# Kernel tuning notes

Hardware: AMD Instinct MI355X
Metric: run time of the kernel (lower is better)

Reference implementation:

```python
import jax, jax.numpy as jnp
import numpy as np

B, C_IN, C_OUT, N, T = 16, 32, 64, 1024, 24
IN_DIM, S_DIM, D_DIM, K, KT = 1, 16, 16, 3, 3


def conv1x1(x, W, b):
    # x: [B,Ci,N,T], W: [Co,Ci], b: [Co] -> [B,Co,N,T]
    return jnp.einsum('oi,bint->bont', W, x) + b[None, :, None, None]


def conv_t(x, W, b):
    # temporal conv, kernel (1,KT), padding (0,1) -> length preserved
    out = jax.lax.conv_general_dilated(
        x, W, window_strides=(1, 1), padding=((0, 0), (1, 1)),
        dimension_numbers=('NCHW', 'OIHW', 'NCHW'))
    return out + b[None, :, None, None]


def coss_attn(Dv, y, Wq, bq, Wk, bk, Wv, bv):
    # cross-attention per node over the temporal axis: Q from y, K/V from Dv
    Q = conv1x1(y, Wq, bq)
    Kx = conv1x1(Dv, Wk, bk)
    V = conv1x1(Dv, Wv, bv)
    scale = 1.0 / jnp.sqrt(jnp.asarray(Q.shape[1], Q.dtype))
    A = jax.nn.softmax(jnp.einsum('bcnt,bcns->bnts', Q, Kx) * scale, axis=-1)
    return jnp.einsum('bnts,bcns->bcnt', A, V)


def cheby(x, supports, Wg, bg, k):
    # Chebyshev polynomial graph conv: T0=I, T1=L, T2=2L T1 - T0
    n = supports.shape[0]
    L0 = jnp.eye(n, dtype=x.dtype)
    L1 = supports
    Ls = [L0, L1]
    for _ in range(2, k):
        L2 = 2.0 * supports @ L1 - L0
        L0, L1 = L1, L2
        Ls.append(L2)
    Lap = jnp.stack(Ls, 0)  # [K,N,N]
    xk = jnp.einsum('kqn,bcnt->bckqt', Lap, x)  # aggregate neighbours
    bsz, c, kk, nn, tt = xk.shape
    xk = xk.reshape(bsz, c * kk, nn, tt)
    return conv1x1(xk, Wg, bg)


def setup_inputs() -> dict:
    key = jax.random.key(0)
    ks = jax.random.split(key, 32)
    s = 0.05
    inp = {
        'x': jax.random.normal(ks[0], (B, C_IN, N, T), jnp.float32),
        'supports': jax.random.normal(ks[1], (N, N), jnp.float32) / np.sqrt(N).astype(np.float32),
        'CD': jax.random.normal(ks[2], (N, D_DIM), jnp.float32),
        'CS': jax.random.normal(ks[3], (N, S_DIM), jnp.float32),
        'adj': jax.random.normal(ks[4], (N, N), jnp.float32) / np.sqrt(N).astype(np.float32),
        # DelayEstimators params
        'W_de': jax.random.normal(ks[5], (C_OUT, C_IN), jnp.float32) * s,
        'b_de': jnp.zeros((C_OUT,), jnp.float32),
        'Wd': jax.random.normal(ks[6], (D_DIM, T), jnp.float32) * s,
        # conv_pro
        'W_pro': jax.random.normal(ks[7], (IN_DIM, C_IN), jnp.float32) * s,
        'b_pro': jnp.zeros((IN_DIM,), jnp.float32),
        # MultiScaleGCN
        'W_mii': jax.random.normal(ks[8], (C_OUT, S_DIM), jnp.float32) * s,
        'b_mii': jnp.zeros((C_OUT,), jnp.float32),
        # conv_1 residual
        'W_1': jax.random.normal(ks[9], (C_OUT, C_IN), jnp.float32) * s,
        'b_1': jnp.zeros((C_OUT,), jnp.float32),
        # TSFN cross-attention (query from x with c_in channels)
        'Wq_t': jax.random.normal(ks[10], (C_OUT, C_IN), jnp.float32) * s,
        'bq_t': jnp.zeros((C_OUT,), jnp.float32),
        'Wk_t': jax.random.normal(ks[11], (C_OUT, C_OUT), jnp.float32) * s,
        'bk_t': jnp.zeros((C_OUT,), jnp.float32),
        'Wv_t': jax.random.normal(ks[12], (C_OUT, C_OUT), jnp.float32) * s,
        'bv_t': jnp.zeros((C_OUT,), jnp.float32),
        # conv1 temporal (1,Kt)
        'W_c1': jax.random.normal(ks[13], (C_OUT, C_OUT, 1, KT), jnp.float32) * s,
        'b_c1': jnp.zeros((C_OUT,), jnp.float32),
        # SSFN cross-attention
        'Wq_s': jax.random.normal(ks[14], (C_OUT, C_OUT), jnp.float32) * s,
        'bq_s': jnp.zeros((C_OUT,), jnp.float32),
        'Wk_s': jax.random.normal(ks[15], (C_OUT, C_OUT), jnp.float32) * s,
        'bk_s': jnp.zeros((C_OUT,), jnp.float32),
        'Wv_s': jax.random.normal(ks[16], (C_OUT, C_OUT), jnp.float32) * s,
        'bv_s': jnp.zeros((C_OUT,), jnp.float32),
        # cheby conv output projection (K*c_out -> 2*c_out)
        'W_g': jax.random.normal(ks[17], (2 * C_OUT, K * C_OUT), jnp.float32) * s,
        'b_g': jnp.zeros((2 * C_OUT,), jnp.float32),
    }
    return inp


def reference(x, supports, CD, CS, adj, W_de, b_de, Wd, W_pro, b_pro,
              W_mii, b_mii, W_1, b_1, Wq_t, bq_t, Wk_t, bk_t, Wv_t, bv_t,
              W_c1, b_c1, Wq_s, bq_s, Wk_s, bk_s, Wv_s, bv_s, W_g, b_g):
    # DelayEstimators: projected trend modulated by node-wise learned delay gate
    delay = jax.nn.sigmoid(jnp.tanh(CD @ Wd))            # [N,T]
    D = conv1x1(x, W_de, b_de) * delay[None, None, :, :]  # [B,c_out,N,T]
    # conv_pro + broadcast of spatial context CS
    u = conv1x1(x, W_pro, b_pro)[:, 0]                    # [B,N,T] (in_dim==1)
    CSb = jnp.einsum('bnt,ne->bent', u, CS)               # [B,S_dim,N,T]
    # MultiScaleGCN: 1x1 projection + adjacency aggregation (identity + adj)
    h = conv1x1(CSb, W_mii, b_mii)
    S = h + jnp.einsum('nm,bcmt->bcnt', adj, h)           # [B,c_out,N,T]
    x_input1 = conv1x1(x, W_1, b_1)
    XD = coss_attn(D, x, Wq_t, bq_t, Wk_t, bk_t, Wv_t, bv_t) + x_input1
    x1 = conv_t(XD, W_c1, b_c1)
    XS = coss_attn(S, x1, Wq_s, bq_s, Wk_s, bk_s, Wv_s, bv_s)
    x2 = cheby(XS, supports, W_g, b_g, K)                 # [B,2*c_out,N,T]
    filt, gate = x2[:, :C_OUT], x2[:, C_OUT:]
    return (filt + x_input1) * jax.nn.sigmoid(gate)
```

## Files before the change

### kernel.cpp

```cpp
#include <hip/hip_runtime.h>
#include <cstdint>
#include <cstddef>

#define B_    16
#define CIN_  32
#define COUT_ 64
#define N_    1024
#define T_    24
#define SD_   16
#define DD_   16

#define NT_      (N_*T_)
#define BNT_     (B_*N_*T_)
#define UE_COLS  (B_*T_*SD_)
#define XS_COLS  (B_*COUT_*T_)
#define HALF_COLS (XS_COLS/2)

typedef unsigned short ushort_t;
using bf16x8 = __attribute__((ext_vector_type(8))) short;
using f32x4  = __attribute__((ext_vector_type(4))) float;

#define OFF_DELAY 0ul
#define OFF_M     98304ul
#define OFF_R     360448ul
#define OFF_U     364544ul
#define OFF_W1T   1953792ul
#define OFF_WGBF  2048000ul
#define OFF_WGT   2097152ul
#define OFF_SBF   2195456ul
#define OFF_ADJBF 4292608ul
#define OFF_STBF  6389760ul
#define OFF_L2BF  8486912ul
#define OFF_X1    10584064ul
#define OFF_X2    23166976ul
#define OFF_XS    48332800ul
#define OFF_Y1H   98664448ul
#define OFF_Y2H   123830272ul
#define OFF_WBF   148996096ul

#define WB_DE   0
#define WB_QT   2048
#define WB_1    4096
#define WB_MIIA 6144
#define WB_KT   8192
#define WB_VT   12288
#define WB_QS   16384
#define WB_KS   20480
#define WB_VS   24576
#define WB_C1A  28672
#define WB_TOTAL 40960

__device__ __forceinline__ float bfb2f(ushort_t h) {
  union { unsigned u; float f; } v; v.u = ((unsigned)h) << 16; return v.f;
}
__device__ __forceinline__ ushort_t f2bfb(float f) {
  union { float f; unsigned u; } v; v.f = f;
  unsigned u = v.u;
  return (ushort_t)((u + 0x7fffu + ((u >> 16) & 1u)) >> 16);
}
__device__ __forceinline__ float sigm_(float z) { return 1.f / (1.f + expf(-z)); }

__device__ __forceinline__ void gl_lds16(const ushort_t* g, ushort_t* l) {
  __builtin_amdgcn_global_load_lds(
      (const __attribute__((address_space(1))) unsigned int*)g,
      (__attribute__((address_space(3))) unsigned int*)l, 16, 0, 0);
}

__device__ __forceinline__ void st4bf(ushort_t* p, float v0, float v1, float v2, float v3) {
  uint2 w;
  w.x = (unsigned)f2bfb(v0) | ((unsigned)f2bfb(v1) << 16);
  w.y = (unsigned)f2bfb(v2) | ((unsigned)f2bfb(v3) << 16);
  *(uint2*)p = w;
}

__global__ __launch_bounds__(256) void k_prep(
    const float* __restrict__ supports, const float* __restrict__ adj,
    const float* __restrict__ W_de, const float* __restrict__ Wq_t,
    const float* __restrict__ W_1, const float* __restrict__ W_mii,
    const float* __restrict__ Wk_t, const float* __restrict__ Wv_t,
    const float* __restrict__ Wq_s, const float* __restrict__ Wk_s,
    const float* __restrict__ Wv_s, const float* __restrict__ W_c1,
    const float* __restrict__ W_g,
    ushort_t* __restrict__ Sbf, ushort_t* __restrict__ adjbf,
    ushort_t* __restrict__ STbf,
    float* __restrict__ W1T, ushort_t* __restrict__ WGBF,
    ushort_t* __restrict__ WBF)
{
  int idx = blockIdx.x * 256 + threadIdx.x;
  if (idx < N_*N_) {
    Sbf[idx]   = f2bfb(supports[idx]);
    adjbf[idx] = f2bfb(adj[idx]);
    int n = idx >> 10, k = idx & 1023;
    STbf[idx]  = f2bfb(supports[k*N_ + n]);
  }
  int j = idx - N_*N_;
  if (j < 0) return;
  if (j < 2048) { int k = j>>6, c = j&63; W1T[j] = W_1[c*32 + k]; return; }
  j -= 2048;
  if (j < 24576) { WGBF[j] = f2bfb(W_g[j]); return; }
  j -= 24576;
  if (j < 2048) { WBF[WB_DE + j] = f2bfb(W_de[j]); return; }
  j -= 2048;
  if (j < 2048) { WBF[WB_QT + j] = f2bfb(Wq_t[j]); return; }
  j -= 2048;
  if (j < 2048) { WBF[WB_1 + j] = f2bfb(W_1[j]); return; }
  j -= 2048;
  if (j < 2048) { int c = j>>5, k = j&31;
                  WBF[WB_MIIA + j] = (k < 16) ? f2bfb(W_mii[c*16 + k]) : (ushort_t)0; return; }
  j -= 2048;
  if (j < 4096) { WBF[WB_KT + j] = f2bfb(Wk_t[j]); return; }
  j -= 4096;
  if (j < 4096) { WBF[WB_VT + j] = f2bfb(Wv_t[j]); return; }
  j -= 4096;
  if (j < 4096) { WBF[WB_QS + j] = f2bfb(Wq_s[j]); return; }
  j -= 4096;
  if (j < 4096) { WBF[WB_KS + j] = f2bfb(Wk_s[j]); return; }
  j -= 4096;
  if (j < 4096) { WBF[WB_VS + j] = f2bfb(Wv_s[j]); return; }
  j -= 4096;
  if (j < 12288) { int d = j >> 12, r = j & 4095, c = r >> 6, jj = r & 63;
                   WBF[WB_C1A + j] = f2bfb(W_c1[(c*64 + jj)*3 + d]); return; }
}
#define PREP_TOTAL (N_*N_ + 2048 + 24576 + WB_TOTAL)

__global__ __launch_bounds__(256) void k_pre(
    const float* __restrict__ CD, const float* __restrict__ Wd,
    const float* __restrict__ CS, const float* __restrict__ W_mii,
    const float* __restrict__ adj,
    float* __restrict__ delay, float* __restrict__ Mbuf, float* __restrict__ Rbuf)
{
  int idx = blockIdx.x * 256 + threadIdx.x;
  if (idx < NT_) {
    int n = idx / T_, t = idx % T_;
    float z = 0.f;
    #pragma unroll
    for (int d = 0; d < DD_; ++d) z += CD[n*DD_ + d] * Wd[d*T_ + t];
    delay[idx] = sigm_(tanhf(z));
  }
  int i2 = idx - NT_;
  if (i2 >= 0 && i2 < N_*COUT_) {
    int n = i2 / COUT_, c = i2 % COUT_;
    float z = 0.f;
    #pragma unroll
    for (int e = 0; e < SD_; ++e) z += CS[n*SD_ + e] * W_mii[c*SD_ + e];
    Mbuf[i2] = z;
  }
  int i3 = idx - NT_ - N_*COUT_;
  if (i3 >= 0 && i3 < N_) {
    const float* row = adj + (size_t)i3 * N_;
    float s = 0.f;
    for (int m = 0; m < N_; ++m) s += row[m];
    Rbuf[i3] = s;
  }
}

__global__ __launch_bounds__(256) void k_u(
    const float* __restrict__ x, const float* __restrict__ W_pro,
    const float* __restrict__ b_pro, const float* __restrict__ CS,
    float* __restrict__ u, ushort_t* __restrict__ Ue)
{
  int idx = blockIdx.x * 256 + threadIdx.x;
  if (idx >= BNT_) return;
  int t = idx % T_;
  int n = (idx / T_) % N_;
  int b = idx / (T_ * N_);
  const float* xp = x + ((size_t)b * CIN_ * N_ + n) * T_ + t;
  float z = b_pro[0];
  #pragma unroll
  for (int i = 0; i < CIN_; ++i) z += W_pro[i] * xp[(size_t)i * NT_];
  u[idx] = z;
  ushort_t* up = Ue + (size_t)n * UE_COLS + (b * T_ + t) * SD_;
  #pragma unroll
  for (int e = 0; e < SD_; ++e) up[e] = f2bfb(z * CS[n*SD_ + e]);
}

__global__ __launch_bounds__(256) void k_tr(
    const ushort_t* __restrict__ src, ushort_t* __restrict__ dst,
    int R, int sstride)
{
  __shared__ ushort_t tb[32][33];
  const int tid = threadIdx.x;
  const int tx = tid & 31, ty = tid >> 5;
  const int c0 = blockIdx.x * 32, r0 = blockIdx.y * 32;
  #pragma unroll
  for (int p = 0; p < 4; ++p) {
    int r = r0 + ty + p*8;
    tb[ty + p*8][tx] = src[(size_t)r * sstride + c0 + tx];
  }
  __syncthreads();
  #pragma unroll
  for (int p = 0; p < 4; ++p) {
    int c = c0 + ty + p*8;
    dst[(size_t)c * R + r0 + tx] = tb[tx][ty + p*8];
  }
}

template<int MODE>
__global__ __launch_bounds__(256) void k_mmx(
    const ushort_t* __restrict__ Abf, const ushort_t* __restrict__ BT,
    ushort_t* __restrict__ Cc, int ncols)
{
  __shared__ ushort_t As[128*64];
  __shared__ ushort_t Bs[128*64];
  const int tid  = threadIdx.x;
  const int wave = tid >> 6, lane = tid & 63;
  const int row0 = blockIdx.y * 128;
  const int col0 = blockIdx.x * 128;
  const int wm = (wave >> 1) * 64, wn = (wave & 1) * 64;
  const int l15 = lane & 15, quad = lane >> 4, l7 = lane & 7;

  f32x4 acc[4][4];
  #pragma unroll
  for (int i = 0; i < 4; ++i)
    #pragma unroll
    for (int j = 0; j < 4; ++j) acc[i][j] = (f32x4){0.f,0.f,0.f,0.f};

  for (int kb = 0; kb < 1024; kb += 64) {
    #pragma unroll
    for (int p = 0; p < 4; ++p) {
      int chunk = p*256 + tid;
      int r = chunk >> 3, pc = chunk & 7;
      int kc = pc ^ (r & 7);
      gl_lds16(Abf + (size_t)(row0 + r)*1024 + (kb + kc*8), &As[chunk*8]);
    }
    #pragma unroll
    for (int p = 0; p < 4; ++p) {
      int chunk = p*256 + tid;
      int r = chunk >> 3, pc = chunk & 7;
      int kc = pc ^ (r & 7);
      gl_lds16(BT + (size_t)(col0 + r)*1024 + (kb + kc*8), &Bs[chunk*8]);
    }
    __syncthreads();
    #pragma unroll
    for (int kh = 0; kh < 2; ++kh) {
      const int kcb = kh * 4;
      bf16x8 af[4], bfr[4];
      #pragma unroll
      for (int mi = 0; mi < 4; ++mi)
        af[mi] = *(const bf16x8*)&As[(wm + mi*16 + l15)*64 + (((kcb + quad) ^ l7) << 3)];
      #pragma unroll
      for (int ni = 0; ni < 4; ++ni)
        bfr[ni] = *(const bf16x8*)&Bs[(wn + ni*16 + l15)*64 + (((kcb + quad) ^ l7) << 3)];
      #pragma unroll
      for (int mi = 0; mi < 4; ++mi)
        #pragma unroll
        for (int ni = 0; ni < 4; ++ni)
          acc[mi][ni] = __builtin_amdgcn_mfma_f32_16x16x32_bf16(
              af[mi], bfr[ni], acc[mi][ni], 0, 0, 0);
    }
    __syncthreads();
  }

  #pragma unroll
  for (int mi = 0; mi < 4; ++mi) {
    int grow_b = row0 + wm + mi*16 + quad*4;
    #pragma unroll
    for (int ni = 0; ni < 4; ++ni) {
      int gcol = col0 + wn + ni*16 + l15;
      #pragma unroll
      for (int j = 0; j < 4; ++j) {
        float v = acc[mi][ni][j];
        int grow = grow_b + j;
        if (MODE == 2) v = 2.f*v - ((grow == gcol) ? 1.f : 0.f);
        Cc[(size_t)grow * ncols + gcol] = f2bfb(v);
      }
    }
  }
}

#define SW 72
__global__ __launch_bounds__(256) void k_attn_mfma(
    const float* __restrict__ x,
    const float* __restrict__ delay, const float* __restrict__ Mbuf,
    const float* __restrict__ Rbuf, const float* __restrict__ u,
    const ushort_t* __restrict__ P,
    const ushort_t* __restrict__ WBF,
    const float* __restrict__ b_de, const float* __restrict__ bq_t,
    const float* __restrict__ b_1,  const float* __restrict__ b_mii,
    const float* __restrict__ bk_t, const float* __restrict__ bv_t,
    const float* __restrict__ bq_s, const float* __restrict__ bk_s,
    const float* __restrict__ bv_s, const float* __restrict__ b_c1,
    ushort_t* __restrict__ XS)
{
  const int n = blockIdx.x, b = blockIdx.y;
  const int tid = threadIdx.x, wave = tid >> 6, lane = tid & 63;
  const int l15 = lane & 15, quad = lane >> 4;

  __shared__ __align__(16) char smem[31520];
  ushort_t* bufQ = (ushort_t*)(smem + 0);
  ushort_t* XDg  = (ushort_t*)(smem + 0);
  ushort_t* Bc   = (ushort_t*)(smem + 4896);
  ushort_t* bufK = (ushort_t*)(smem + 4896);
  ushort_t* scb  = (ushort_t*)(smem + 4896);
  ushort_t* Pts  = (ushort_t*)(smem + 9504);
  float*    scf  = (float*)(smem + 9504);
  ushort_t* bufD = (ushort_t*)(smem + 12064);
  ushort_t* x1s  = (ushort_t*)(smem + 16672);
  ushort_t* Sts  = (ushort_t*)(smem + 21280);
  ushort_t* V2   = (ushort_t*)(smem + 25888);
  float* delay_s = (float*)(smem + 31008);
  float* urow    = (float*)(smem + 31136);
  float* Mrow    = (float*)(smem + 31264);

  for (int i = tid; i < 768; i += 256) {
    int ci = i / 24, t = i - ci*24;
    Bc[t*SW + ci] = f2bfb(x[(((size_t)b*CIN_ + ci)*N_ + n)*T_ + t]);
  }
  for (int i = tid; i < 768; i += 256) {
    int t = i >> 5, e = i & 31;
    Pts[t*40 + e] = (e < 16) ? P[(size_t)n*UE_COLS + (b*T_ + t)*SD_ + e] : (ushort_t)0;
  }
  if (tid < 32)       urow[tid] = (tid < 24) ? u[((size_t)b*N_ + n)*T_ + tid] : 0.f;
  else if (tid < 64)  { int t = tid - 32; delay_s[t] = (t < 24) ? delay[n*T_ + t] : 0.f; }
  else if (tid < 128) Mrow[tid - 64] = Mbuf[n*COUT_ + (tid - 64)];
  for (int i = tid; i < 64*40; i += 256) V2[i] = 0;
  __syncthreads();

  const int c0 = wave * 16;
  const float Rn = Rbuf[n];

  {
    bf16x8 aD = *(const bf16x8*)(WBF + WB_DE   + (c0+l15)*32 + quad*8);
    bf16x8 aQ = *(const bf16x8*)(WBF + WB_QT   + (c0+l15)*32 + quad*8);
    bf16x8 a1 = *(const bf16x8*)(WBF + WB_1    + (c0+l15)*32 + quad*8);
    bf16x8 aS = *(const bf16x8*)(WBF + WB_MIIA + (c0+l15)*32 + quad*8);
    float4 bD4 = *(const float4*)&b_de [c0 + quad*4];
    float4 bQ4 = *(const float4*)&bq_t [c0 + quad*4];
    float4 b14 = *(const float4*)&b_1  [c0 + quad*4];
    float4 bS4 = *(const float4*)&b_mii[c0 + quad*4];
    float4 Mv4 = *(const float4*)&Mrow [c0 + quad*4];
    float bD[4] = {bD4.x,bD4.y,bD4.z,bD4.w};
    float bQ[4] = {bQ4.x,bQ4.y,bQ4.z,bQ4.w};
    float b1a[4] = {b14.x,b14.y,b14.z,b14.w};
    float bS[4] = {bS4.x,bS4.y,bS4.z,bS4.w};
    float Mv[4] = {Mv4.x,Mv4.y,Mv4.z,Mv4.w};
    #pragma unroll
    for (int nt = 0; nt < 2; ++nt) {
      int bt = nt*16 + l15;
      bf16x8 bx = *(const bf16x8*)&Bc[bt*SW + quad*8];
      bf16x8 bp = *(const bf16x8*)&Pts[bt*40 + quad*8];
      f32x4 z = {0.f,0.f,0.f,0.f};
      f32x4 accD = __builtin_amdgcn_mfma_f32_16x16x32_bf16(aD, bx, z, 0,0,0);
      f32x4 accQ = __builtin_amdgcn_mfma_f32_16x16x32_bf16(aQ, bx, z, 0,0,0);
      f32x4 acc1 = __builtin_amdgcn_mfma_f32_16x16x32_bf16(a1, bx, z, 0,0,0);
      f32x4 accS = __builtin_amdgcn_mfma_f32_16x16x32_bf16(aS, bp, z, 0,0,0);
      float dl = delay_s[bt], ut = urow[bt];
      st4bf(&bufD[bt*SW + c0 + quad*4],
            (accD[0]+bD[0])*dl, (accD[1]+bD[1])*dl, (accD[2]+bD[2])*dl, (accD[3]+bD[3])*dl);
      st4bf(&bufQ[bt*SW + c0 + quad*4],
            accQ[0]+bQ[0], accQ[1]+bQ[1], accQ[2]+bQ[2], accQ[3]+bQ[3]);
      st4bf(&x1s[bt*SW + c0 + quad*4],
            acc1[0]+b1a[0], acc1[1]+b1a[1], acc1[2]+b1a[2], acc1[3]+b1a[3]);
      st4bf(&Sts[bt*SW + c0 + quad*4],
            accS[0] + ut*Mv[0] + bS[0]*(1.f+Rn), accS[1] + ut*Mv[1] + bS[1]*(1.f+Rn),
            accS[2] + ut*Mv[2] + bS[2]*(1.f+Rn), accS[3] + ut*Mv[3] + bS[3]*(1.f+Rn));
    }
  }
  __syncthreads();

  {
    bf16x8 aK0 = *(const bf16x8*)(WBF + WB_KT + (c0+l15)*64 + quad*8);
    bf16x8 aK1 = *(const bf16x8*)(WBF + WB_KT + (c0+l15)*64 + 32 + quad*8);
    bf16x8 aV0 = *(const bf16x8*)(WBF + WB_VT + (c0+l15)*64 + quad*8);
    bf16x8 aV1 = *(const bf16x8*)(WBF + WB_VT + (c0+l15)*64 + 32 + quad*8);
    float4 bK4 = *(const float4*)&bk_t[c0 + quad*4];
    float4 bV4 = *(const float4*)&bv_t[c0 + quad*4];
    float bK[4] = {bK4.x,bK4.y,bK4.z,bK4.w};
    float bV[4] = {bV4.x,bV4.y,bV4.z,bV4.w};
    #pragma unroll
    for (int nt = 0; nt < 2; ++nt) {
      int bt = nt*16 + l15;
      bf16x8 b0 = *(const bf16x8*)&bufD[bt*SW + quad*8];
      bf16x8 b1v = *(const bf16x8*)&bufD[bt*SW + 32 + quad*8];
      f32x4 accK = {0.f,0.f,0.f,0.f}, accV = {0.f,0.f,0.f,0.f};
      accK = __builtin_amdgcn_mfma_f32_16x16x32_bf16(aK0, b0,  accK, 0,0,0);
      accK = __builtin_amdgcn_mfma_f32_16x16x32_bf16(aK1, b1v, accK, 0,0,0);
      accV = __builtin_amdgcn_mfma_f32_16x16x32_bf16(aV0, b0,  accV, 0,0,0);
      accV = __builtin_amdgcn_mfma_f32_16x16x32_bf16(aV1, b1v, accV, 0,0,0);
      st4bf(&bufK[bt*SW + c0 + quad*4],
            accK[0]+bK[0], accK[1]+bK[1], accK[2]+bK[2], accK[3]+bK[3]);
      if (bt < 24) {
        #pragma unroll
        for (int r = 0; r < 4; ++r)
          V2[(c0 + quad*4 + r)*40 + bt] = f2bfb(accV[r] + bV[r]);
      }
    }
  }
  __syncthreads();

  {
    int mt = (wave >> 1) * 16, ns = (wave & 1) * 16;
    bf16x8 a0 = *(const bf16x8*)&bufQ[(mt+l15)*SW + quad*8];
    bf16x8 a1f = *(const bf16x8*)&bufQ[(mt+l15)*SW + 32 + quad*8];
    bf16x8 b0 = *(const bf16x8*)&bufK[(ns+l15)*SW + quad*8];
    bf16x8 b1f = *(const bf16x8*)&bufK[(ns+l15)*SW + 32 + quad*8];
    f32x4 acc = {0.f,0.f,0.f,0.f};
    acc = __builtin_amdgcn_mfma_f32_16x16x32_bf16(a0, b0, acc, 0,0,0);
    acc = __builtin_amdgcn_mfma_f32_16x16x32_bf16(a1f, b1f, acc, 0,0,0);
    int s = ns + l15;
    if (s < 24) {
      #pragma unroll
      for (int r = 0; r < 4; ++r) {
        int t = mt + quad*4 + r;
        if (t < 24) scf[t*25 + s] = 0.125f * acc[r];
      }
    }
  }
  __syncthreads();

  {
    int t = tid >> 3, j = tid & 7;
    if (t < 24) {
      float v0 = scf[t*25 + j], v1 = scf[t*25 + j + 8], v2 = scf[t*25 + j + 16];
      float mx = fmaxf(fmaxf(v0, v1), v2);
      mx = fmaxf(mx, __shfl_xor(mx, 1));
      mx = fmaxf(mx, __shfl_xor(mx, 2));
      mx = fmaxf(mx, __shfl_xor(mx, 4));
      float e0 = expf(v0 - mx), e1 = expf(v1 - mx), e2 = expf(v2 - mx);
      float sm = e0 + e1 + e2;
      sm += __shfl_xor(sm, 1);
      sm += __shfl_xor(sm, 2);
      sm += __shfl_xor(sm, 4);
      float inv = 1.f / sm;
      scb[t*40 + j]      = f2bfb(e0 * inv);
      scb[t*40 + j + 8]  = f2bfb(e1 * inv);
      scb[t*40 + j + 16] = f2bfb(e2 * inv);
      scb[t*40 + 24 + j] = 0;
    }
  }
  __syncthreads();

  {
    for (int i = tid; i < 640; i += 256) {
      int r = i >> 6, cg = i & 63;
      int row = (r == 0) ? 0 : (24 + r);
      XDg[row*SW + cg] = 0;
    }
    int nc = wave * 16;
    bf16x8 bv0 = *(const bf16x8*)&V2[(nc + l15)*40 + quad*8];
    #pragma unroll
    for (int mt = 0; mt < 2; ++mt) {
      bf16x8 af = *(const bf16x8*)&scb[(mt*16 + l15)*40 + quad*8];
      f32x4 acc = {0.f,0.f,0.f,0.f};
      acc = __builtin_amdgcn_mfma_f32_16x16x32_bf16(af, bv0, acc, 0,0,0);
      int ccol = nc + l15;
      #pragma unroll
      for (int r = 0; r < 4; ++r) {
        int t = mt*16 + quad*4 + r;
        if (t < 24)
          XDg[(1 + t)*SW + ccol] = f2bfb(acc[r] + bfb2f(x1s[t*SW + ccol]));
      }
    }
  }
  __syncthreads();

  {
    float4 bc4 = *(const float4*)&b_c1[c0 + quad*4];
    float bc[4] = {bc4.x,bc4.y,bc4.z,bc4.w};
    f32x4 acc0 = {0.f,0.f,0.f,0.f}, acc1v = {0.f,0.f,0.f,0.f};
    #pragma unroll
    for (int d = 0; d < 3; ++d) {
      const ushort_t* Ad = WBF + WB_C1A + d*4096;
      bf16x8 a0 = *(const bf16x8*)(Ad + (c0+l15)*64 + quad*8);
      bf16x8 a1f = *(const bf16x8*)(Ad + (c0+l15)*64 + 32 + quad*8);
      {
        int rr = 0*16 + l15 + d;
        bf16x8 b0 = *(const bf16x8*)&XDg[rr*SW + quad*8];
        bf16x8 b1f = *(const bf16x8*)&XDg[rr*SW + 32 + quad*8];
        acc0 = __builtin_amdgcn_mfma_f32_16x16x32_bf16(a0, b0, acc0, 0,0,0);
        acc0 = __builtin_amdgcn_mfma_f32_16x16x32_bf16(a1f, b1f, acc0, 0,0,0);
      }
      {
        int rr = 1*16 + l15 + d;
        bf16x8 b0 = *(const bf16x8*)&XDg[rr*SW + quad*8];
        bf16x8 b1f = *(const bf16x8*)&XDg[rr*SW + 32 + quad*8];
        acc1v = __builtin_amdgcn_mfma_f32_16x16x32_bf16(a0, b0, acc1v, 0,0,0);
        acc1v = __builtin_amdgcn_mfma_f32_16x16x32_bf16(a1f, b1f, acc1v, 0,0,0);
      }
    }
    st4bf(&bufD[(0*16 + l15)*SW + c0 + quad*4],
          acc0[0]+bc[0], acc0[1]+bc[1], acc0[2]+bc[2], acc0[3]+bc[3]);
    st4bf(&bufD[(1*16 + l15)*SW + c0 + quad*4],
          acc1v[0]+bc[0], acc1v[1]+bc[1], acc1v[2]+bc[2], acc1v[3]+bc[3]);
  }
  __syncthreads();

  {
    bf16x8 aq0 = *(const bf16x8*)(WBF + WB_QS + (c0+l15)*64 + quad*8);
    bf16x8 aq1 = *(const bf16x8*)(WBF + WB_QS + (c0+l15)*64 + 32 + quad*8);
    bf16x8 ak0 = *(const bf16x8*)(WBF + WB_KS + (c0+l15)*64 + quad*8);
    bf16x8 ak1 = *(const bf16x8*)(WBF + WB_KS + (c0+l15)*64 + 32 + quad*8);
    bf16x8 av0 = *(const bf16x8*)(WBF + WB_VS + (c0+l15)*64 + quad*8);
    bf16x8 av1 = *(const bf16x8*)(WBF + WB_VS + (c0+l15)*64 + 32 + quad*8);
    float4 bq4 = *(const float4*)&bq_s[c0 + quad*4];
    float4 bk4 = *(const float4*)&bk_s[c0 + quad*4];
    float4 bv4 = *(const float4*)&bv_s[c0 + quad*4];
    float bq[4] = {bq4.x,bq4.y,bq4.z,bq4.w};
    float bk[4] = {bk4.x,bk4.y,bk4.z,bk4.w};
    float bv[4] = {bv4.x,bv4.y,bv4.z,bv4.w};
    #pragma unroll
    for (int nt = 0; nt < 2; ++nt) {
      int bt = nt*16 + l15;
      bf16x8 bx0 = *(const bf16x8*)&bufD[bt*SW + quad*8];
      bf16x8 bx1 = *(const bf16x8*)&bufD[bt*SW + 32 + quad*8];
      bf16x8 bs0 = *(const bf16x8*)&Sts[bt*SW + quad*8];
      bf16x8 bs1 = *(const bf16x8*)&Sts[bt*SW + 32 + quad*8];
      f32x4 accQ = {0.f,0.f,0.f,0.f}, accK = {0.f,0.f,0.f,0.f}, accV = {0.f,0.f,0.f,0.f};
      accQ = __builtin_amdgcn_mfma_f32_16x16x32_bf16(aq0, bx0, accQ, 0,0,0);
      accQ = __builtin_amdgcn_mfma_f32_16x16x32_bf16(aq1, bx1, accQ, 0,0,0);
      accK = __builtin_amdgcn_mfma_f32_16x16x32_bf16(ak0, bs0, accK, 0,0,0);
      accK = __builtin_amdgcn_mfma_f32_16x16x32_bf16(ak1, bs1, accK, 0,0,0);
      accV = __builtin_amdgcn_mfma_f32_16x16x32_bf16(av0, bs0, accV, 0,0,0);
      accV = __builtin_amdgcn_mfma_f32_16x16x32_bf16(av1, bs1, accV, 0,0,0);
      st4bf(&bufQ[bt*SW + c0 + quad*4],
            accQ[0]+bq[0], accQ[1]+bq[1], accQ[2]+bq[2], accQ[3]+bq[3]);
      st4bf(&bufK[bt*SW + c0 + quad*4],
            accK[0]+bk[0], accK[1]+bk[1], accK[2]+bk[2], accK[3]+bk[3]);
      if (bt < 24) {
        #pragma unroll
        for (int r = 0; r < 4; ++r)
          V2[(c0 + quad*4 + r)*40 + bt] = f2bfb(accV[r] + bv[r]);
      }
    }
  }
  __syncthreads();

  {
    int mt = (wave >> 1) * 16, ns = (wave & 1) * 16;
    bf16x8 a0 = *(const bf16x8*)&bufQ[(mt+l15)*SW + quad*8];
    bf16x8 a1f = *(const bf16x8*)&bufQ[(mt+l15)*SW + 32 + quad*8];
    bf16x8 b0 = *(const bf16x8*)&bufK[(ns+l15)*SW + quad*8];
    bf16x8 b1f = *(const bf16x8*)&bufK[(ns+l15)*SW + 32 + quad*8];
    f32x4 acc = {0.f,0.f,0.f,0.f};
    acc = __builtin_amdgcn_mfma_f32_16x16x32_bf16(a0, b0, acc, 0,0,0);
    acc = __builtin_amdgcn_mfma_f32_16x16x32_bf16(a1f, b1f, acc, 0,0,0);
    int s = ns + l15;
    if (s < 24) {
      #pragma unroll
      for (int r = 0; r < 4; ++r) {
        int t = mt + quad*4 + r;
        if (t < 24) scf[t*25 + s] = 0.125f * acc[r];
      }
    }
  }
  __syncthreads();

  {
    int t = tid >> 3, j = tid & 7;
    if (t < 24) {
      float v0 = scf[t*25 + j], v1 = scf[t*25 + j + 8], v2 = scf[t*25 + j + 16];
      float mx = fmaxf(fmaxf(v0, v1), v2);
      mx = fmaxf(mx, __shfl_xor(mx, 1));
      mx = fmaxf(mx, __shfl_xor(mx, 2));
      mx = fmaxf(mx, __shfl_xor(mx, 4));
      float e0 = expf(v0 - mx), e1 = expf(v1 - mx), e2 = expf(v2 - mx);
      float sm = e0 + e1 + e2;
      sm += __shfl_xor(sm, 1);
      sm += __shfl_xor(sm, 2);
      sm += __shfl_xor(sm, 4);
      float inv = 1.f / sm;
      scb[t*40 + j]      = f2bfb(e0 * inv);
      scb[t*40 + j + 8]  = f2bfb(e1 * inv);
      scb[t*40 + j + 16] = f2bfb(e2 * inv);
      scb[t*40 + 24 + j] = 0;
    }
  }
  __syncthreads();

  {
    int nc = wave * 16;
    bf16x8 bv0 = *(const bf16x8*)&V2[(nc + l15)*40 + quad*8];
    #pragma unroll
    for (int mt = 0; mt < 2; ++mt) {
      bf16x8 af = *(const bf16x8*)&scb[(mt*16 + l15)*40 + quad*8];
      f32x4 acc = {0.f,0.f,0.f,0.f};
      acc = __builtin_amdgcn_mfma_f32_16x16x32_bf16(af, bv0, acc, 0,0,0);
      int ccol = nc + l15;
      int t0 = mt*16 + quad*4;
      if (t0 < 24) {
        uint2 w;
        w.x = (unsigned)f2bfb(acc[0]) | ((unsigned)f2bfb(acc[1]) << 16);
        w.y = (unsigned)f2bfb(acc[2]) | ((unsigned)f2bfb(acc[3]) << 16);
        *(uint2*)(XS + (size_t)n*XS_COLS + (size_t)b*COUT_*T_ + ccol*T_ + t0) = w;
      }
    }
  }
}

#define ZW 200
__global__ __launch_bounds__(256) void k_final(
    const float* __restrict__ x,
    const ushort_t* __restrict__ XS, const ushort_t* __restrict__ Y1h,
    const ushort_t* __restrict__ Y2h,
    const ushort_t* __restrict__ WGBF,
    const float* __restrict__ W1T, const float* __restrict__ b_1,
    const float* __restrict__ b_g,
    int h, float* __restrict__ out)
{
  const int n = blockIdx.x, bb = blockIdx.y, tid = threadIdx.x;
  const int b = h * 8 + bb;
  const int wave = tid >> 6, lane = tid & 63;
  const int l15 = lane & 15, quad = lane >> 4;

  __shared__ __align__(16) ushort_t Zt[32*ZW];
  __shared__ float x1sh[COUT_*T_];
  __shared__ float xts[CIN_*T_];

  size_t baseg = (size_t)n * XS_COLS + (size_t)b * COUT_ * T_;
  size_t baseh = (size_t)n * HALF_COLS + (size_t)bb * COUT_ * T_;

  for (int i = tid; i < 8*ZW; i += 256) Zt[24*ZW + i] = 0;
  for (int i = tid; i < COUT_*T_; i += 256) {
    int c = i / T_, t = i - c*T_;
    ushort_t* zr = &Zt[t*ZW + 3*c];
    zr[0] = XS [baseg + i];
    zr[1] = Y1h[baseh + i];
    zr[2] = Y2h[baseh + i];
  }
  for (int i = tid; i < CIN_*T_; i += 256) {
    int ci = i / T_, t = i - ci*T_;
    xts[i] = x[(((size_t)b * CIN_ + ci) * N_ + n) * T_ + t];
  }
  __syncthreads();

  {
    const int c = tid >> 2, tq = tid & 3;
    float a[6];
    #pragma unroll
    for (int m = 0; m < 6; ++m) a[m] = b_1[c];
    for (int i = 0; i < CIN_; ++i) {
      float w = W1T[i*64 + c];
      #pragma unroll
      for (int m = 0; m < 6; ++m) a[m] += w * xts[i*T_ + tq + 4*m];
    }
    #pragma unroll
    for (int m = 0; m < 6; ++m) x1sh[c*T_ + tq + 4*m] = a[m];
  }

  f32x4 accF[2] = {{0.f,0.f,0.f,0.f},{0.f,0.f,0.f,0.f}};
  f32x4 accG[2] = {{0.f,0.f,0.f,0.f},{0.f,0.f,0.f,0.f}};
  const ushort_t* WF = WGBF + (size_t)(wave*16 + l15)*192 + quad*8;
  const ushort_t* WG = WF + 64*192;
  #pragma unroll
  for (int ks = 0; ks < 6; ++ks) {
    bf16x8 wf = *(const bf16x8*)(WF + ks*32);
    bf16x8 wg = *(const bf16x8*)(WG + ks*32);
    #pragma unroll
    for (int nt = 0; nt < 2; ++nt) {
      bf16x8 bz = *(const bf16x8*)&Zt[(nt*16 + l15)*ZW + ks*32 + quad*8];
      accF[nt] = __builtin_amdgcn_mfma_f32_16x16x32_bf16(wf, bz, accF[nt], 0,0,0);
      accG[nt] = __builtin_amdgcn_mfma_f32_16x16x32_bf16(wg, bz, accG[nt], 0,0,0);
    }
  }
  __syncthreads();

  {
    float4 bgF4 = *(const float4*)&b_g[wave*16 + quad*4];
    float4 bgG4 = *(const float4*)&b_g[64 + wave*16 + quad*4];
    float bgF[4] = {bgF4.x, bgF4.y, bgF4.z, bgF4.w};
    float bgG[4] = {bgG4.x, bgG4.y, bgG4.z, bgG4.w};
    #pragma unroll
    for (int nt = 0; nt < 2; ++nt) {
      int t = nt*16 + l15;
      if (t < 24) {
        #pragma unroll
        for (int r = 0; r < 4; ++r) {
          int c = wave*16 + quad*4 + r;
          float fv = accF[nt][r] + bgF[r] + x1sh[c*T_ + t];
          float gv = accG[nt][r] + bgG[r];
          out[(((size_t)b * COUT_ + c) * N_ + n) * T_ + t] = fv * sigm_(gv);
        }
      }
    }
  }
}

extern "C" void kernel_launch(void* const* d_in, const int* in_sizes, int n_in,
                              void* d_out, int out_size, void* d_ws, size_t ws_size,
                              hipStream_t stream) {
  const float* x        = (const float*)d_in[0];
  const float* supports = (const float*)d_in[1];
  const float* CD       = (const float*)d_in[2];
  const float* CS       = (const float*)d_in[3];
  const float* adj      = (const float*)d_in[4];
  const float* W_de  = (const float*)d_in[5];  const float* b_de  = (const float*)d_in[6];
  const float* Wd    = (const float*)d_in[7];
  const float* W_pro = (const float*)d_in[8];  const float* b_pro = (const float*)d_in[9];
  const float* W_mii = (const float*)d_in[10]; const float* b_mii = (const float*)d_in[11];
  const float* W_1   = (const float*)d_in[12]; const float* b_1   = (const float*)d_in[13];
  const float* Wq_t  = (const float*)d_in[14]; const float* bq_t  = (const float*)d_in[15];
  const float* Wk_t  = (const float*)d_in[16]; const float* bk_t  = (const float*)d_in[17];
  const float* Wv_t  = (const float*)d_in[18]; const float* bv_t  = (const float*)d_in[19];
  const float* W_c1  = (const float*)d_in[20]; const float* b_c1  = (const float*)d_in[21];
  const float* Wq_s  = (const float*)d_in[22]; const float* bq_s  = (const float*)d_in[23];
  const float* Wk_s  = (const float*)d_in[24]; const float* bk_s  = (const float*)d_in[25];
  const float* Wv_s  = (const float*)d_in[26]; const float* bv_s  = (const float*)d_in[27];
  const float* W_g   = (const float*)d_in[28]; const float* b_g   = (const float*)d_in[29];
  float* out = (float*)d_out;

  char* ws = (char*)d_ws;
  float*    delay = (float*)(ws + OFF_DELAY);
  float*    Mbuf  = (float*)(ws + OFF_M);
  float*    Rbuf  = (float*)(ws + OFF_R);
  float*    u     = (float*)(ws + OFF_U);
  float*    W1T   = (float*)(ws + OFF_W1T);
  ushort_t* WGBF  = (ushort_t*)(ws + OFF_WGBF);
  ushort_t* Sbf   = (ushort_t*)(ws + OFF_SBF);
  ushort_t* adjbf = (ushort_t*)(ws + OFF_ADJBF);
  ushort_t* STbf  = (ushort_t*)(ws + OFF_STBF);
  ushort_t* L2bf  = (ushort_t*)(ws + OFF_L2BF);
  ushort_t* Ue    = (ushort_t*)(ws + OFF_X1);
  ushort_t* P     = (ushort_t*)(ws + OFF_X1);
  ushort_t* UeT   = (ushort_t*)(ws + OFF_X2);
  ushort_t* XST   = (ushort_t*)(ws + OFF_X2);
  ushort_t* XS    = (ushort_t*)(ws + OFF_XS);
  ushort_t* Y1h   = (ushort_t*)(ws + OFF_Y1H);
  ushort_t* Y2h   = (ushort_t*)(ws + OFF_Y2H);
  ushort_t* WBF   = (ushort_t*)(ws + OFF_WBF);

  (void)in_sizes; (void)n_in; (void)out_size; (void)ws_size;

  k_prep<<<dim3((PREP_TOTAL + 255)/256), 256, 0, stream>>>(
      supports, adj, W_de, Wq_t, W_1, W_mii, Wk_t, Wv_t, Wq_s, Wk_s, Wv_s,
      W_c1, W_g, Sbf, adjbf, STbf, W1T, WGBF, WBF);
  k_pre<<<dim3((NT_ + N_*COUT_ + N_ + 255)/256), 256, 0, stream>>>(
      CD, Wd, CS, W_mii, adj, delay, Mbuf, Rbuf);
  k_mmx<2><<<dim3(8, 8), 256, 0, stream>>>(Sbf, STbf, L2bf, 1024);
  k_u<<<dim3((BNT_ + 255)/256), 256, 0, stream>>>(x, W_pro, b_pro, CS, u, Ue);
  k_tr<<<dim3(UE_COLS/32, N_/32), 256, 0, stream>>>(Ue, UeT, N_, UE_COLS);
  k_mmx<0><<<dim3(UE_COLS/128, N_/128), 256, 0, stream>>>(adjbf, UeT, P, UE_COLS);
  k_attn_mfma<<<dim3(N_, B_), 256, 0, stream>>>(
      x, delay, Mbuf, Rbuf, u, P, WBF,
      b_de, bq_t, b_1, b_mii, bk_t, bv_t, bq_s, bk_s, bv_s, b_c1, XS);
  for (int h = 0; h < 2; ++h) {
    k_tr<<<dim3(HALF_COLS/32, N_/32), 256, 0, stream>>>(
        XS + (size_t)h * HALF_COLS, XST, N_, XS_COLS);
    k_mmx<0><<<dim3(HALF_COLS/128, N_/128), 256, 0, stream>>>(Sbf, XST, Y1h, HALF_COLS);
    k_mmx<0><<<dim3(HALF_COLS/128, N_/128), 256, 0, stream>>>(L2bf, XST, Y2h, HALF_COLS);
    k_final<<<dim3(N_, 8), 256, 0, stream>>>(
        x, XS, Y1h, Y2h, WGBF, W1T, b_1, b_g, h, out);
  }
}
```

Measured before the change: 799.9 us.

## Merge Chebyshev GEMMs, restructure attention softmax in registers, shrink LDS footprint

The two per-half Chebyshev GEMMs (S and L2 against XST) are merged into one launch, with grid.y choosing the A matrix, which cuts launches and improves tail fill. Both attention stages now compute the 24x24 scores in two waves with the softmax done in registers via shuffles, removing an fp32 score buffer in shared memory and one barrier. The x_input1 term is held in registers instead of LDS, and the shared buffers are re-aliased so each block uses less LDS, with launch bounds raised to allow more resident blocks. The supports transpose moves from a strided gather in prep to the existing tiled transpose kernel, and the adj row sums are split across 8 lanes. Risks are more register pressure and two idle waves during the score step.

```diff
diff --git a/kernel.cpp b/kernel.cpp
--- a/kernel.cpp
+++ b/kernel.cpp
@@ -26,7 +26,6 @@
 #define OFF_U     364544ul
 #define OFF_W1T   1953792ul
 #define OFF_WGBF  2048000ul
-#define OFF_WGT   2097152ul
 #define OFF_SBF   2195456ul
 #define OFF_ADJBF 4292608ul
 #define OFF_STBF  6389760ul
@@ -82,7 +81,6 @@
     const float* __restrict__ Wv_s, const float* __restrict__ W_c1,
     const float* __restrict__ W_g,
     ushort_t* __restrict__ Sbf, ushort_t* __restrict__ adjbf,
-    ushort_t* __restrict__ STbf,
     float* __restrict__ W1T, ushort_t* __restrict__ WGBF,
     ushort_t* __restrict__ WBF)
 {
@@ -90,8 +88,6 @@
   if (idx < N_*N_) {
     Sbf[idx]   = f2bfb(supports[idx]);
     adjbf[idx] = f2bfb(adj[idx]);
-    int n = idx >> 10, k = idx & 1023;
-    STbf[idx]  = f2bfb(supports[k*N_ + n]);
   }
   int j = idx - N_*N_;
   if (j < 0) return;
@@ -146,11 +142,15 @@
     Mbuf[i2] = z;
   }
   int i3 = idx - NT_ - N_*COUT_;
-  if (i3 >= 0 && i3 < N_) {
-    const float* row = adj + (size_t)i3 * N_;
+  if (i3 >= 0 && i3 < 8*N_) {
+    int n = i3 >> 3, jl = i3 & 7;
+    const float* row = adj + (size_t)n * N_;
     float s = 0.f;
-    for (int m = 0; m < N_; ++m) s += row[m];
-    Rbuf[i3] = s;
+    for (int m = jl; m < N_; m += 8) s += row[m];
+    s += __shfl_xor(s, 1);
+    s += __shfl_xor(s, 2);
+    s += __shfl_xor(s, 4);
+    if (jl == 0) Rbuf[n] = s;
   }
 }
 
@@ -268,8 +268,80 @@
   }
 }
 
+__global__ __launch_bounds__(256) void k_mmy(
+    const ushort_t* __restrict__ Sbf, const ushort_t* __restrict__ L2bf,
+    const ushort_t* __restrict__ BT,
+    ushort_t* __restrict__ Y1, ushort_t* __restrict__ Y2, int ncols)
+{
+  __shared__ ushort_t As[128*64];
+  __shared__ ushort_t Bs[128*64];
+  const int tid  = threadIdx.x;
+  const int wave = tid >> 6, lane = tid & 63;
+  const bool isY2 = blockIdx.y >= 8;
+  const ushort_t* Abf = isY2 ? L2bf : Sbf;
+  ushort_t* Cc = isY2 ? Y2 : Y1;
+  const int row0 = (blockIdx.y & 7) * 128;
+  const int col0 = blockIdx.x * 128;
+  const int wm = (wave >> 1) * 64, wn = (wave & 1) * 64;
+  const int l15 = lane & 15, quad = lane >> 4, l7 = lane & 7;
+
+  f32x4 acc[4][4];
+  #pragma unroll
+  for (int i = 0; i < 4; ++i)
+    #pragma unroll
+    for (int j = 0; j < 4; ++j) acc[i][j] = (f32x4){0.f,0.f,0.f,0.f};
+
+  for (int kb = 0; kb < 1024; kb += 64) {
+    #pragma unroll
+    for (int p = 0; p < 4; ++p) {
+      int chunk = p*256 + tid;
+      int r = chunk >> 3, pc = chunk & 7;
+      int kc = pc ^ (r & 7);
+      gl_lds16(Abf + (size_t)(row0 + r)*1024 + (kb + kc*8), &As[chunk*8]);
+    }
+    #pragma unroll
+    for (int p = 0; p < 4; ++p) {
+      int chunk = p*256 + tid;
+      int r = chunk >> 3, pc = chunk & 7;
+      int kc = pc ^ (r & 7);
+      gl_lds16(BT + (size_t)(col0 + r)*1024 + (kb + kc*8), &Bs[chunk*8]);
+    }
+    __syncthreads();
+    #pragma unroll
+    for (int kh = 0; kh < 2; ++kh) {
+      const int kcb = kh * 4;
+      bf16x8 af[4], bfr[4];
+      #pragma unroll
+      for (int mi = 0; mi < 4; ++mi)
+        af[mi] = *(const bf16x8*)&As[(wm + mi*16 + l15)*64 + (((kcb + quad) ^ l7) << 3)];
+      #pragma unroll
+      for (int ni = 0; ni < 4; ++ni)
+        bfr[ni] = *(const bf16x8*)&Bs[(wn + ni*16 + l15)*64 + (((kcb + quad) ^ l7) << 3)];
+      #pragma unroll
+      for (int mi = 0; mi < 4; ++mi)
+        #pragma unroll
+        for (int ni = 0; ni < 4; ++ni)
+          acc[mi][ni] = __builtin_amdgcn_mfma_f32_16x16x32_bf16(
+              af[mi], bfr[ni], acc[mi][ni], 0, 0, 0);
+    }
+    __syncthreads();
+  }
+
+  #pragma unroll
+  for (int mi = 0; mi < 4; ++mi) {
+    int grow_b = row0 + wm + mi*16 + quad*4;
+    #pragma unroll
+    for (int ni = 0; ni < 4; ++ni) {
+      int gcol = col0 + wn + ni*16 + l15;
+      #pragma unroll
+      for (int j = 0; j < 4; ++j)
+        Cc[(size_t)(grow_b + j) * ncols + gcol] = f2bfb(acc[mi][ni][j]);
+    }
+  }
+}
+
 #define SW 72
-__global__ __launch_bounds__(256) void k_attn_mfma(
+__global__ __launch_bounds__(256, 6) void k_attn_mfma(
     const float* __restrict__ x,
     const float* __restrict__ delay, const float* __restrict__ Mbuf,
     const float* __restrict__ Rbuf, const float* __restrict__ u,
@@ -286,21 +358,19 @@
   const int tid = threadIdx.x, wave = tid >> 6, lane = tid & 63;
   const int l15 = lane & 15, quad = lane >> 4;
 
-  __shared__ __align__(16) char smem[31520];
+  __shared__ __align__(16) char smem[24352];
   ushort_t* bufQ = (ushort_t*)(smem + 0);
   ushort_t* XDg  = (ushort_t*)(smem + 0);
   ushort_t* Bc   = (ushort_t*)(smem + 4896);
   ushort_t* bufK = (ushort_t*)(smem + 4896);
-  ushort_t* scb  = (ushort_t*)(smem + 4896);
-  ushort_t* Pts  = (ushort_t*)(smem + 9504);
-  float*    scf  = (float*)(smem + 9504);
-  ushort_t* bufD = (ushort_t*)(smem + 12064);
-  ushort_t* x1s  = (ushort_t*)(smem + 16672);
-  ushort_t* Sts  = (ushort_t*)(smem + 21280);
-  ushort_t* V2   = (ushort_t*)(smem + 25888);
-  float* delay_s = (float*)(smem + 31008);
-  float* urow    = (float*)(smem + 31136);
-  float* Mrow    = (float*)(smem + 31264);
+  ushort_t* bufD = (ushort_t*)(smem + 9504);
+  ushort_t* scb  = (ushort_t*)(smem + 9504);
+  ushort_t* Sts  = (ushort_t*)(smem + 14112);
+  ushort_t* V2   = (ushort_t*)(smem + 18720);
+  ushort_t* Pts  = (ushort_t*)(smem + 18720);
+  float* delay_s = (float*)(smem + 23840);
+  float* urow    = (float*)(smem + 23968);
+  float* Mrow    = (float*)(smem + 24096);
 
   for (int i = tid; i < 768; i += 256) {
     int ci = i / 24, t = i - ci*24;
@@ -313,16 +383,16 @@
   if (tid < 32)       urow[tid] = (tid < 24) ? u[((size_t)b*N_ + n)*T_ + tid] : 0.f;
   else if (tid < 64)  { int t = tid - 32; delay_s[t] = (t < 24) ? delay[n*T_ + t] : 0.f; }
   else if (tid < 128) Mrow[tid - 64] = Mbuf[n*COUT_ + (tid - 64)];
-  for (int i = tid; i < 64*40; i += 256) V2[i] = 0;
   __syncthreads();
 
   const int c0 = wave * 16;
   const float Rn = Rbuf[n];
+  float x1r[2][4];
 
   {
     bf16x8 aD = *(const bf16x8*)(WBF + WB_DE   + (c0+l15)*32 + quad*8);
     bf16x8 aQ = *(const bf16x8*)(WBF + WB_QT   + (c0+l15)*32 + quad*8);
-    bf16x8 a1 = *(const bf16x8*)(WBF + WB_1    + (c0+l15)*32 + quad*8);
+    bf16x8 a1w = *(const bf16x8*)(WBF + WB_1   + (c0+l15)*32 + quad*8);
     bf16x8 aS = *(const bf16x8*)(WBF + WB_MIIA + (c0+l15)*32 + quad*8);
     float4 bD4 = *(const float4*)&b_de [c0 + quad*4];
     float4 bQ4 = *(const float4*)&bq_t [c0 + quad*4];
@@ -342,15 +412,15 @@
       f32x4 z = {0.f,0.f,0.f,0.f};
       f32x4 accD = __builtin_amdgcn_mfma_f32_16x16x32_bf16(aD, bx, z, 0,0,0);
       f32x4 accQ = __builtin_amdgcn_mfma_f32_16x16x32_bf16(aQ, bx, z, 0,0,0);
-      f32x4 acc1 = __builtin_amdgcn_mfma_f32_16x16x32_bf16(a1, bx, z, 0,0,0);
+      f32x4 acc1 = __builtin_amdgcn_mfma_f32_16x16x32_bf16(a1w, bx, z, 0,0,0);
       f32x4 accS = __builtin_amdgcn_mfma_f32_16x16x32_bf16(aS, bp, z, 0,0,0);
       float dl = delay_s[bt], ut = urow[bt];
       st4bf(&bufD[bt*SW + c0 + quad*4],
             (accD[0]+bD[0])*dl, (accD[1]+bD[1])*dl, (accD[2]+bD[2])*dl, (accD[3]+bD[3])*dl);
       st4bf(&bufQ[bt*SW + c0 + quad*4],
             accQ[0]+bQ[0], accQ[1]+bQ[1], accQ[2]+bQ[2], accQ[3]+bQ[3]);
-      st4bf(&x1s[bt*SW + c0 + quad*4],
-            acc1[0]+b1a[0], acc1[1]+b1a[1], acc1[2]+b1a[2], acc1[3]+b1a[3]);
+      #pragma unroll
+      for (int r = 0; r < 4; ++r) x1r[nt][r] = acc1[r] + b1a[r];
       st4bf(&Sts[bt*SW + c0 + quad*4],
             accS[0] + ut*Mv[0] + bS[0]*(1.f+Rn), accS[1] + ut*Mv[1] + bS[1]*(1.f+Rn),
             accS[2] + ut*Mv[2] + bS[2]*(1.f+Rn), accS[3] + ut*Mv[3] + bS[3]*(1.f+Rn));
@@ -359,6 +429,7 @@
   __syncthreads();
 
   {
+    for (int i = tid; i < 512; i += 256) V2[(i>>3)*40 + 24 + (i&7)] = 0;
     bf16x8 aK0 = *(const bf16x8*)(WBF + WB_KT + (c0+l15)*64 + quad*8);
     bf16x8 aK1 = *(const bf16x8*)(WBF + WB_KT + (c0+l15)*64 + 32 + quad*8);
     bf16x8 aV0 = *(const bf16x8*)(WBF + WB_VT + (c0+l15)*64 + quad*8);
@@ -388,44 +459,40 @@
   }
   __syncthreads();
 
-  {
-    int mt = (wave >> 1) * 16, ns = (wave & 1) * 16;
+  if (wave < 2) {
+    const int mt = wave * 16;
     bf16x8 a0 = *(const bf16x8*)&bufQ[(mt+l15)*SW + quad*8];
     bf16x8 a1f = *(const bf16x8*)&bufQ[(mt+l15)*SW + 32 + quad*8];
-    bf16x8 b0 = *(const bf16x8*)&bufK[(ns+l15)*SW + quad*8];
-    bf16x8 b1f = *(const bf16x8*)&bufK[(ns+l15)*SW + 32 + quad*8];
-    f32x4 acc = {0.f,0.f,0.f,0.f};
-    acc = __builtin_amdgcn_mfma_f32_16x16x32_bf16(a0, b0, acc, 0,0,0);
-    acc = __builtin_amdgcn_mfma_f32_16x16x32_bf16(a1f, b1f, acc, 0,0,0);
-    int s = ns + l15;
-    if (s < 24) {
-      #pragma unroll
-      for (int r = 0; r < 4; ++r) {
-        int t = mt + quad*4 + r;
-        if (t < 24) scf[t*25 + s] = 0.125f * acc[r];
-      }
-    }
-  }
-  __syncthreads();
-
-  {
-    int t = tid >> 3, j = tid & 7;
-    if (t < 24) {
-      float v0 = scf[t*25 + j], v1 = scf[t*25 + j + 8], v2 = scf[t*25 + j + 16];
-      float mx = fmaxf(fmaxf(v0, v1), v2);
+    bf16x8 k0a = *(const bf16x8*)&bufK[l15*SW + quad*8];
+    bf16x8 k0b = *(const bf16x8*)&bufK[l15*SW + 32 + quad*8];
+    bf16x8 k1a = *(const bf16x8*)&bufK[(16+l15)*SW + quad*8];
+    bf16x8 k1b = *(const bf16x8*)&bufK[(16+l15)*SW + 32 + quad*8];
+    f32x4 s0 = {0.f,0.f,0.f,0.f}, s1 = {0.f,0.f,0.f,0.f};
+    s0 = __builtin_amdgcn_mfma_f32_16x16x32_bf16(a0, k0a, s0, 0,0,0);
+    s0 = __builtin_amdgcn_mfma_f32_16x16x32_bf16(a1f, k0b, s0, 0,0,0);
+    s1 = __builtin_amdgcn_mfma_f32_16x16x32_bf16(a0, k1a, s1, 0,0,0);
+    s1 = __builtin_amdgcn_mfma_f32_16x16x32_bf16(a1f, k1b, s1, 0,0,0);
+    #pragma unroll
+    for (int r = 0; r < 4; ++r) {
+      float v0 = 0.125f * s0[r];
+      float v1 = (l15 < 8) ? 0.125f * s1[r] : -3.0e38f;
+      float mx = fmaxf(v0, v1);
       mx = fmaxf(mx, __shfl_xor(mx, 1));
       mx = fmaxf(mx, __shfl_xor(mx, 2));
       mx = fmaxf(mx, __shfl_xor(mx, 4));
-      float e0 = expf(v0 - mx), e1 = expf(v1 - mx), e2 = expf(v2 - mx);
-      float sm = e0 + e1 + e2;
+      mx = fmaxf(mx, __shfl_xor(mx, 8));
+      float e0 = expf(v0 - mx);
+      float e1 = (l15 < 8) ? expf(v1 - mx) : 0.f;
+      float sm = e0 + e1;
       sm += __shfl_xor(sm, 1);
       sm += __shfl_xor(sm, 2);
       sm += __shfl_xor(sm, 4);
+      sm += __shfl_xor(sm, 8);
       float inv = 1.f / sm;
-      scb[t*40 + j]      = f2bfb(e0 * inv);
-      scb[t*40 + j + 8]  = f2bfb(e1 * inv);
-      scb[t*40 + j + 16] = f2bfb(e2 * inv);
-      scb[t*40 + 24 + j] = 0;
+      int t = mt + quad*4 + r;
+      bool tv = (t < 24);
+      scb[t*40 + l15]      = tv ? f2bfb(e0 * inv) : (ushort_t)0;
+      scb[t*40 + 16 + l15] = (tv && l15 < 8) ? f2bfb(e1 * inv) : (ushort_t)0;
     }
   }
   __syncthreads();
@@ -436,19 +503,17 @@
       int row = (r == 0) ? 0 : (24 + r);
       XDg[row*SW + cg] = 0;
     }
-    int nc = wave * 16;
-    bf16x8 bv0 = *(const bf16x8*)&V2[(nc + l15)*40 + quad*8];
-    #pragma unroll
-    for (int mt = 0; mt < 2; ++mt) {
-      bf16x8 af = *(const bf16x8*)&scb[(mt*16 + l15)*40 + quad*8];
-      f32x4 acc = {0.f,0.f,0.f,0.f};
-      acc = __builtin_amdgcn_mfma_f32_16x16x32_bf16(af, bv0, acc, 0,0,0);
-      int ccol = nc + l15;
-      #pragma unroll
-      for (int r = 0; r < 4; ++r) {
-        int t = mt*16 + quad*4 + r;
-        if (t < 24)
-          XDg[(1 + t)*SW + ccol] = f2bfb(acc[r] + bfb2f(x1s[t*SW + ccol]));
+    bf16x8 aV = *(const bf16x8*)&V2[(c0 + l15)*40 + quad*8];
+    #pragma unroll
+    for (int nt = 0; nt < 2; ++nt) {
+      bf16x8 bP = *(const bf16x8*)&scb[(nt*16 + l15)*40 + quad*8];
+      f32x4 z = {0.f,0.f,0.f,0.f};
+      f32x4 acc = __builtin_amdgcn_mfma_f32_16x16x32_bf16(aV, bP, z, 0,0,0);
+      int t = nt*16 + l15;
+      if (t < 24) {
+        #pragma unroll
+        for (int r = 0; r < 4; ++r)
+          XDg[(1 + t)*SW + c0 + quad*4 + r] = f2bfb(acc[r] + x1r[nt][r]);
       }
     }
   }
@@ -525,44 +590,40 @@
   }
   __syncthreads();
 
-  {
-    int mt = (wave >> 1) * 16, ns = (wave & 1) * 16;
+  if (wave < 2) {
+    const int mt = wave * 16;
     bf16x8 a0 = *(const bf16x8*)&bufQ[(mt+l15)*SW + quad*8];
     bf16x8 a1f = *(const bf16x8*)&bufQ[(mt+l15)*SW + 32 + quad*8];
-    bf16x8 b0 = *(const bf16x8*)&bufK[(ns+l15)*SW + quad*8];
-    bf16x8 b1f = *(const bf16x8*)&bufK[(ns+l15)*SW + 32 + quad*8];
-    f32x4 acc = {0.f,0.f,0.f,0.f};
-    acc = __builtin_amdgcn_mfma_f32_16x16x32_bf16(a0, b0, acc, 0,0,0);
-    acc = __builtin_amdgcn_mfma_f32_16x16x32_bf16(a1f, b1f, acc, 0,0,0);
-    int s = ns + l15;
-    if (s < 24) {
-      #pragma unroll
-      for (int r = 0; r < 4; ++r) {
-        int t = mt + quad*4 + r;
-        if (t < 24) scf[t*25 + s] = 0.125f * acc[r];
-      }
-    }
-  }
-  __syncthreads();
-
-  {
-    int t = tid >> 3, j = tid & 7;
-    if (t < 24) {
-      float v0 = scf[t*25 + j], v1 = scf[t*25 + j + 8], v2 = scf[t*25 + j + 16];
-      float mx = fmaxf(fmaxf(v0, v1), v2);
+    bf16x8 k0a = *(const bf16x8*)&bufK[l15*SW + quad*8];
+    bf16x8 k0b = *(const bf16x8*)&bufK[l15*SW + 32 + quad*8];
+    bf16x8 k1a = *(const bf16x8*)&bufK[(16+l15)*SW + quad*8];
+    bf16x8 k1b = *(const bf16x8*)&bufK[(16+l15)*SW + 32 + quad*8];
+    f32x4 s0 = {0.f,0.f,0.f,0.f}, s1 = {0.f,0.f,0.f,0.f};
+    s0 = __builtin_amdgcn_mfma_f32_16x16x32_bf16(a0, k0a, s0, 0,0,0);
+    s0 = __builtin_amdgcn_mfma_f32_16x16x32_bf16(a1f, k0b, s0, 0,0,0);
+    s1 = __builtin_amdgcn_mfma_f32_16x16x32_bf16(a0, k1a, s1, 0,0,0);
+    s1 = __builtin_amdgcn_mfma_f32_16x16x32_bf16(a1f, k1b, s1, 0,0,0);
+    #pragma unroll
+    for (int r = 0; r < 4; ++r) {
+      float v0 = 0.125f * s0[r];
+      float v1 = (l15 < 8) ? 0.125f * s1[r] : -3.0e38f;
+      float mx = fmaxf(v0, v1);
       mx = fmaxf(mx, __shfl_xor(mx, 1));
       mx = fmaxf(mx, __shfl_xor(mx, 2));
       mx = fmaxf(mx, __shfl_xor(mx, 4));
-      float e0 = expf(v0 - mx), e1 = expf(v1 - mx), e2 = expf(v2 - mx);
-      float sm = e0 + e1 + e2;
+      mx = fmaxf(mx, __shfl_xor(mx, 8));
+      float e0 = expf(v0 - mx);
+      float e1 = (l15 < 8) ? expf(v1 - mx) : 0.f;
+      float sm = e0 + e1;
       sm += __shfl_xor(sm, 1);
       sm += __shfl_xor(sm, 2);
       sm += __shfl_xor(sm, 4);
+      sm += __shfl_xor(sm, 8);
       float inv = 1.f / sm;
-      scb[t*40 + j]      = f2bfb(e0 * inv);
-      scb[t*40 + j + 8]  = f2bfb(e1 * inv);
-      scb[t*40 + j + 16] = f2bfb(e2 * inv);
-      scb[t*40 + 24 + j] = 0;
+      int t = mt + quad*4 + r;
+      bool tv = (t < 24);
+      scb[t*40 + l15]      = tv ? f2bfb(e0 * inv) : (ushort_t)0;
+      scb[t*40 + 16 + l15] = (tv && l15 < 8) ? f2bfb(e1 * inv) : (ushort_t)0;
     }
   }
   __syncthreads();
@@ -573,8 +634,8 @@
     #pragma unroll
     for (int mt = 0; mt < 2; ++mt) {
       bf16x8 af = *(const bf16x8*)&scb[(mt*16 + l15)*40 + quad*8];
-      f32x4 acc = {0.f,0.f,0.f,0.f};
-      acc = __builtin_amdgcn_mfma_f32_16x16x32_bf16(af, bv0, acc, 0,0,0);
+      f32x4 z = {0.f,0.f,0.f,0.f};
+      f32x4 acc = __builtin_amdgcn_mfma_f32_16x16x32_bf16(af, bv0, z, 0,0,0);
       int ccol = nc + l15;
       int t0 = mt*16 + quad*4;
       if (t0 < 24) {
@@ -722,9 +783,10 @@
 
   k_prep<<<dim3((PREP_TOTAL + 255)/256), 256, 0, stream>>>(
       supports, adj, W_de, Wq_t, W_1, W_mii, Wk_t, Wv_t, Wq_s, Wk_s, Wv_s,
-      W_c1, W_g, Sbf, adjbf, STbf, W1T, WGBF, WBF);
-  k_pre<<<dim3((NT_ + N_*COUT_ + N_ + 255)/256), 256, 0, stream>>>(
+      W_c1, W_g, Sbf, adjbf, W1T, WGBF, WBF);
+  k_pre<<<dim3((NT_ + N_*COUT_ + 8*N_ + 255)/256), 256, 0, stream>>>(
       CD, Wd, CS, W_mii, adj, delay, Mbuf, Rbuf);
+  k_tr<<<dim3(N_/32, N_/32), 256, 0, stream>>>(Sbf, STbf, N_, N_);
   k_mmx<2><<<dim3(8, 8), 256, 0, stream>>>(Sbf, STbf, L2bf, 1024);
   k_u<<<dim3((BNT_ + 255)/256), 256, 0, stream>>>(x, W_pro, b_pro, CS, u, Ue);
   k_tr<<<dim3(UE_COLS/32, N_/32), 256, 0, stream>>>(Ue, UeT, N_, UE_COLS);
@@ -735,8 +797,8 @@
   for (int h = 0; h < 2; ++h) {
     k_tr<<<dim3(HALF_COLS/32, N_/32), 256, 0, stream>>>(
         XS + (size_t)h * HALF_COLS, XST, N_, XS_COLS);
-    k_mmx<0><<<dim3(HALF_COLS/128, N_/128), 256, 0, stream>>>(Sbf, XST, Y1h, HALF_COLS);
-    k_mmx<0><<<dim3(HALF_COLS/128, N_/128), 256, 0, stream>>>(L2bf, XST, Y2h, HALF_COLS);
+    k_mmy<<<dim3(HALF_COLS/128, 16), 256, 0, stream>>>(
+        Sbf, L2bf, XST, Y1h, Y2h, HALF_COLS);
     k_final<<<dim3(N_, 8), 256, 0, stream>>>(
         x, XS, Y1h, Y2h, WGBF, W1T, b_1, b_g, h, out);
   }
```

New measurement: 775.4 us. 1.03x faster.
